# Optimization experiments

Measured on AMD Instinct MI355X. Metric: run time of the kernel, lower is better.

## Reference

```python
import jax, jax.numpy as jnp
import numpy as np

B, H, P, D, NF = 16, 16, 128, 128, 12  # patches == head_dim required by lin_qk


def setup_inputs() -> dict:
    key = jax.random.key(0)
    ks = jax.random.split(key, 8)
    return {
        "q": jax.random.normal(ks[0], (B, H, P, D), jnp.float32),
        "k": jax.random.normal(ks[1], (B, H, P, D), jnp.float32),
        "scale": jnp.ones((1,), jnp.float32),  # unused by the original forward
        "grid": jnp.arange(NF, dtype=jnp.float32) + 1.0,
        "base_weight": jax.random.uniform(ks[2], (D, D), jnp.float32),
        "coef_q": jax.random.uniform(ks[3], (D, NF), jnp.float32),
        "coef_k": jax.random.uniform(ks[4], (D, NF), jnp.float32),
        "scale_base": jnp.ones((1, H, P, D), jnp.float32),
        "scale_sp": jnp.ones((1, H, P, D), jnp.float32),
        "w_qk": jax.random.normal(ks[5], (D, D), jnp.float32) / np.float32(np.sqrt(D)),
        "b_qk": jnp.zeros((D,), jnp.float32),
    }


def _branch(x, coef, grid, base_weight, scale_sp, scale_base):
    # base path: SiLU(x) @ W^T  (F.linear semantics)
    base = jax.nn.silu(x) @ base_weight.T
    # KAN sin basis: sin(grid_f * x_d) -> (B,H,P,NF,D); contract coef[d,f]
    s = jnp.sin(grid[:, None] * x[..., None, :])
    f = jnp.einsum('df,bhpfd->bhpd', coef, s)
    return jax.nn.sigmoid(f * scale_sp + base * scale_base)


def reference(q, k, scale, grid, base_weight, coef_q, coef_k, scale_base, scale_sp, w_qk, b_qk):
    # Per-channel sigmoids, then sum over D. The original builds the full
    # (B,H,P,P,D) broadcast tensor sig_q[...,p,None,:] + sig_k[...,None,p',:]
    # and sums over D; that is exactly separable:
    #   sum_d(sig_q[p,d]) + sum_d(sig_k[p',d])
    sq = _branch(q, coef_q, grid, base_weight, scale_sp, scale_base).sum(-1)  # (B,H,P)
    sk = _branch(k, coef_k, grid, base_weight, scale_sp, scale_base).sum(-1)  # (B,H,P)
    f_out = sq[..., :, None] + sk[..., None, :]  # (B,H,P,P)
    f_out = f_out @ w_qk.T + b_qk  # lin_qk: valid because patches == head_dim
    return jax.nn.softmax(f_out, axis=-1)
```

## Files before the change

### kernel.cpp

```cpp
#include <hip/hip_runtime.h>
#include <hip/hip_bf16.h>


typedef float          f32x4 __attribute__((ext_vector_type(4)));
typedef short          s16x8 __attribute__((ext_vector_type(8)));
typedef int            s32x4 __attribute__((ext_vector_type(4)));
typedef unsigned int   u32x4 __attribute__((ext_vector_type(4)));
typedef unsigned short u16x8 __attribute__((ext_vector_type(8)));

#define LOG2E   1.44269504f
#define NLOG2E -1.44269504f
#define INV2PI  0.15915494309189535f

static __device__ __forceinline__ float hw_exp2(float x) {
    float r;
    asm("v_exp_f32 %0, %1" : "=v"(r) : "v"(x));
    return r;
}
static __device__ __forceinline__ float hw_sin_rev(float rev) {
    float f, r;
    asm("v_fract_f32 %0, %1" : "=v"(f) : "v"(rev));
    asm("v_sin_f32 %0, %1" : "=v"(r) : "v"(f));
    return r;
}
static __device__ __forceinline__ float fastrcp(float x) {
    return __builtin_amdgcn_rcpf(x);
}
static __device__ __forceinline__ unsigned int cvt_pk_bf16(float lo, float hi) {
    unsigned int r;
    asm("v_cvt_pk_bf16_f32 %0, %1, %2" : "=v"(r) : "v"(lo), "v"(hi));
    return r;
}
static __device__ __forceinline__ float sigmoid_fast(float z) {
    return fastrcp(1.f + hw_exp2(z * NLOG2E));
}
static __device__ __forceinline__ int swz(int local) {
    return local ^ (((local >> 8) & 7) << 4);
}

__global__ __launch_bounds__(256) void k_convert(const float* __restrict__ bw,
                                                 unsigned short* __restrict__ wbf) {
    int i = blockIdx.x * 256 + threadIdx.x;
    if (i < 128 * 128) {
        __hip_bfloat16 h = __float2bfloat16(bw[i]);
        unsigned short r;
        __builtin_memcpy(&r, &h, 2);
        wbf[i] = r;
    }
}

__global__ __launch_bounds__(512, 4) void k_branch(
    const float* __restrict__ q, const float* __restrict__ k,
    const unsigned short* __restrict__ wbf,
    const float* __restrict__ gridv,
    const float* __restrict__ coef_q, const float* __restrict__ coef_k,
    const float* __restrict__ sbase,
    const float* __restrict__ ssp,
    float* __restrict__ sums_lo, float* __restrict__ sums_hi)
{
    __shared__ char smem[32768];
    float* F_l = (float*)smem;

    const int t = threadIdx.x;
    const int lane = t & 63, w = t >> 6;
    const int wr = w >> 1;
    const int ch = w & 1;
    const int r15 = lane & 15, g4 = lane >> 4;
    const int row0 = blockIdx.x * 64;
    const bool is_q = row0 < 32768;
    const float* X = is_q ? q : k;
    const float* coef = is_q ? coef_q : coef_k;
    const int xrow0 = is_q ? row0 : row0 - 32768;
    const float g1 = gridv[0];

    #pragma unroll
    for (int it = 0; it < 4; ++it) {
        int c = it * 512 + t;
        u16x8 v = *(const u16x8*)&wbf[c * 8];
        *(u16x8*)(smem + swz(c * 16)) = v;
    }
    __syncthreads();

    const float* xrowp = &X[(xrow0 + wr * 16 + r15) * 128];

    f32x4 acc[4];
    #pragma unroll
    for (int n = 0; n < 4; ++n) acc[n] = (f32x4){0.f, 0.f, 0.f, 0.f};

    #pragma unroll
    for (int s = 0; s < 4; ++s) {
        const float4* xp = (const float4*)&xrowp[s * 32 + g4 * 8];
        float4 x0 = xp[0], x1 = xp[1];
        float xsv[8] = {x0.x, x0.y, x0.z, x0.w, x1.x, x1.y, x1.z, x1.w};
        float sl[8];
        #pragma unroll
        for (int j = 0; j < 8; ++j) {
            float e = hw_exp2(xsv[j] * NLOG2E);
            sl[j] = xsv[j] * fastrcp(1.f + e);
        }
        s32x4 a4 = {(int)cvt_pk_bf16(sl[0], sl[1]), (int)cvt_pk_bf16(sl[2], sl[3]),
                    (int)cvt_pk_bf16(sl[4], sl[5]), (int)cvt_pk_bf16(sl[6], sl[7])};
        s16x8 af = __builtin_bit_cast(s16x8, a4);
        #pragma unroll
        for (int n = 0; n < 4; ++n) {
            s16x8 bf = *(const s16x8*)(smem + swz((ch * 64 + n * 16 + r15) * 256
                                                  + s * 64 + g4 * 16));
            acc[n] = __builtin_amdgcn_mfma_f32_16x16x32_bf16(af, bf, acc[n], 0, 0, 0);
        }
    }
    __syncthreads();

    #pragma unroll
    for (int n = 0; n < 4; ++n) {
        int cl = n * 16 + r15;
        #pragma unroll
        for (int reg = 0; reg < 4; ++reg) {
            int rl = g4 * 4 + reg;
            F_l[(wr * 16 + rl) * 128 + ch * 64 + ((cl + rl * 4) & 63)] = acc[n][reg];
        }
    }

    const int ce = lane & 15;
    const int re = lane >> 4;
    const int gcol = ch * 64 + ce * 4;

    float Fr[16], xr[16], spr[16], sbr[16];
    #pragma unroll
    for (int i = 0; i < 4; ++i) {
        int rl = re * 4 + i;
        int rb = wr * 16 + rl;
        int hp = (row0 + rb) & 2047;
        f32x4 F4 = *(f32x4*)&F_l[rb * 128 + ch * 64 + ((ce * 4 + rl * 4) & 63)];
        float4 x4 = *(const float4*)&X[(xrow0 + rb) * 128 + gcol];
        float4 sp = *(const float4*)&ssp[hp * 128 + gcol];
        float4 sb = *(const float4*)&sbase[hp * 128 + gcol];
        Fr[i*4+0]=F4[0]; Fr[i*4+1]=F4[1]; Fr[i*4+2]=F4[2]; Fr[i*4+3]=F4[3];
        xr[i*4+0]=x4.x;  xr[i*4+1]=x4.y;  xr[i*4+2]=x4.z;  xr[i*4+3]=x4.w;
        spr[i*4+0]=sp.x; spr[i*4+1]=sp.y; spr[i*4+2]=sp.z; spr[i*4+3]=sp.w;
        sbr[i*4+0]=sb.x; sbr[i*4+1]=sb.y; sbr[i*4+2]=sb.z; sbr[i*4+3]=sb.w;
    }

    const float grev = g1 * INV2PI;
    float ps[4] = {0.f, 0.f, 0.f, 0.f};
    #pragma unroll
    for (int j = 0; j < 4; ++j) {
        const float4* cp = (const float4*)&coef[(gcol + j) * 12];
        float4 c0 = cp[0], c1 = cp[1], c2 = cp[2];
        float cf[12] = {c0.x, c0.y, c0.z, c0.w, c1.x, c1.y, c1.z, c1.w,
                        c2.x, c2.y, c2.z, c2.w};
        #pragma unroll
        for (int i = 0; i < 4; ++i) {
            float xv = xr[i*4+j];
            float rev = grev * xv;
            float s1 = hw_sin_rev(rev);
            float cv = hw_sin_rev(rev + 0.25f);
            float t2 = cv + cv;
            float sprev = 0.f, scur = s1;
            float f = cf[0] * s1;
            #pragma unroll
            for (int u = 1; u < 12; ++u) {
                float sn = __builtin_fmaf(t2, scur, -sprev);
                f = __builtin_fmaf(cf[u], sn, f);
                sprev = scur; scur = sn;
            }
            float z = f * spr[i*4+j] + Fr[i*4+j] * sbr[i*4+j];
            ps[i] += sigmoid_fast(z);
        }
    }
    #pragma unroll
    for (int i = 0; i < 4; ++i) {
        float v = ps[i];
        v += __shfl_xor(v, 1, 64);
        v += __shfl_xor(v, 2, 64);
        v += __shfl_xor(v, 4, 64);
        v += __shfl_xor(v, 8, 64);
        if (ce == 0) {
            int grow = row0 + wr * 16 + re * 4 + i;
            (ch ? sums_hi : sums_lo)[grow] = v;
        }
    }
}

__global__ __launch_bounds__(256) void k_attn(
    const float* __restrict__ sums_lo, const float* __restrict__ sums_hi,
    const float* __restrict__ w_qk, const float* __restrict__ b_qk,
    float* __restrict__ out)
{
    __shared__ float skl[128], Tp[2][128], Rp[2][128], Tl[128], Rl[128];
    const int bh = blockIdx.x >> 1;
    const int half = blockIdx.x & 1;
    const int t = threadIdx.x;

    if (t < 128) {
        int idx = 32768 + bh * 128 + t;
        skl[t] = sums_lo[idx] + sums_hi[idx];
    }
    __syncthreads();
    {
        int j = t & 127, ph = t >> 7;
        const float4* wr = (const float4*)&w_qk[j * 128 + ph * 64];
        const float* sk2 = &skl[ph * 64];
        float a = 0.f, r = 0.f;
        #pragma unroll 8
        for (int p4 = 0; p4 < 16; ++p4) {
            float4 w4 = wr[p4];
            a += w4.x * sk2[p4 * 4 + 0] + w4.y * sk2[p4 * 4 + 1] +
                 w4.z * sk2[p4 * 4 + 2] + w4.w * sk2[p4 * 4 + 3];
            r += w4.x + w4.y + w4.z + w4.w;
        }
        Tp[ph][j] = a;
        Rp[ph][j] = r;
    }
    __syncthreads();
    if (t < 128) {
        Tl[t] = Tp[0][t] + Tp[1][t] + b_qk[t];
        Rl[t] = Rp[0][t] + Rp[1][t];
    }
    __syncthreads();

    const int lane = t & 63, w = t >> 6;
    #pragma unroll
    for (int it = 0; it < 16; ++it) {
        int row = bh * 128 + half * 64 + it * 4 + w;
        float sqv = sums_lo[row] + sums_hi[row];
        float2 r2 = *(const float2*)&Rl[lane * 2];
        float2 t2 = *(const float2*)&Tl[lane * 2];
        float l0 = __builtin_fmaf(sqv, r2.x, t2.x);
        float l1 = __builtin_fmaf(sqv, r2.y, t2.y);
        float m = fmaxf(l0, l1);
        #pragma unroll
        for (int s = 32; s >= 1; s >>= 1) m = fmaxf(m, __shfl_xor(m, s, 64));
        float e0 = hw_exp2((l0 - m) * LOG2E);
        float e1 = hw_exp2((l1 - m) * LOG2E);
        float sum = e0 + e1;
        #pragma unroll
        for (int w2 = 32; w2 >= 1; w2 >>= 1) sum += __shfl_xor(sum, w2, 64);
        float inv = fastrcp(sum);
        float2 o2 = {e0 * inv, e1 * inv};
        *(float2*)&out[row * 128 + lane * 2] = o2;
    }
}

extern "C" void kernel_launch(void* const* d_in, const int* in_sizes, int n_in,
                              void* d_out, int out_size, void* d_ws, size_t ws_size,
                              hipStream_t stream) {
    (void)in_sizes; (void)n_in; (void)out_size; (void)ws_size;
    const float* q      = (const float*)d_in[0];
    const float* k      = (const float*)d_in[1];
    const float* gridv  = (const float*)d_in[3];
    const float* bw     = (const float*)d_in[4];
    const float* coef_q = (const float*)d_in[5];
    const float* coef_k = (const float*)d_in[6];
    const float* sbase  = (const float*)d_in[7];
    const float* ssp    = (const float*)d_in[8];
    const float* w_qk   = (const float*)d_in[9];
    const float* b_qk   = (const float*)d_in[10];

    float* out  = (float*)d_out;
    float* ws      = (float*)d_ws;
    float* sums_lo = ws;
    float* sums_hi = ws + 65536;
    unsigned short* wbf = (unsigned short*)(ws + 131072);

    k_convert<<<64, 256, 0, stream>>>(bw, wbf);
    k_branch<<<1024, 512, 0, stream>>>(q, k, wbf, gridv, coef_q, coef_k,
                                       sbase, ssp, sums_lo, sums_hi);
    k_attn<<<512, 256, 0, stream>>>(sums_lo, sums_hi, w_qk, b_qk, out);
}
```

Before: 42.83 us.

## Fuse KAN sine basis into MFMA loop using registered x and LDS coefficients

Computes the sine-basis sum during the MFMA loop from x values already held in registers for the SiLU operand, instead of reloading x, coef and scale_sp from global memory in a separate phase. Coefficients are transposed into LDS. The MFMA operands are swapped so the accumulator layout matches per-row ownership. The epilogue now exchanges only the basis values through LDS and uses a two-step shuffle reduction. It also uses v_cos_f32 directly rather than a second fract and sin, at the cost of extra LDS and more register pressure inside the MFMA loop.

```diff
diff --git a/kernel.cpp b/kernel.cpp
--- a/kernel.cpp
+++ b/kernel.cpp
@@ -5,7 +5,6 @@
 typedef float          f32x4 __attribute__((ext_vector_type(4)));
 typedef short          s16x8 __attribute__((ext_vector_type(8)));
 typedef int            s32x4 __attribute__((ext_vector_type(4)));
-typedef unsigned int   u32x4 __attribute__((ext_vector_type(4)));
 typedef unsigned short u16x8 __attribute__((ext_vector_type(8)));
 
 #define LOG2E   1.44269504f
@@ -17,10 +16,19 @@
     asm("v_exp_f32 %0, %1" : "=v"(r) : "v"(x));
     return r;
 }
-static __device__ __forceinline__ float hw_sin_rev(float rev) {
-    float f, r;
-    asm("v_fract_f32 %0, %1" : "=v"(f) : "v"(rev));
+static __device__ __forceinline__ float hw_fract(float x) {
+    float r;
+    asm("v_fract_f32 %0, %1" : "=v"(r) : "v"(x));
+    return r;
+}
+static __device__ __forceinline__ float hw_sin01(float f) {
+    float r;
     asm("v_sin_f32 %0, %1" : "=v"(r) : "v"(f));
+    return r;
+}
+static __device__ __forceinline__ float hw_cos01(float f) {
+    float r;
+    asm("v_cos_f32 %0, %1" : "=v"(r) : "v"(f));
     return r;
 }
 static __device__ __forceinline__ float fastrcp(float x) {
@@ -58,8 +66,8 @@
     const float* __restrict__ ssp,
     float* __restrict__ sums_lo, float* __restrict__ sums_hi)
 {
-    __shared__ char smem[32768];
-    float* F_l = (float*)smem;
+    __shared__ char smem[32768 + 6144];
+    float* cfl = (float*)(smem + 32768);
 
     const int t = threadIdx.x;
     const int lane = t & 63, w = t >> 6;
@@ -72,6 +80,7 @@
     const float* coef = is_q ? coef_q : coef_k;
     const int xrow0 = is_q ? row0 : row0 - 32768;
     const float g1 = gridv[0];
+    const float grev = g1 * INV2PI;
 
     #pragma unroll
     for (int it = 0; it < 4; ++it) {
@@ -79,13 +88,24 @@
         u16x8 v = *(const u16x8*)&wbf[c * 8];
         *(u16x8*)(smem + swz(c * 16)) = v;
     }
-    __syncthreads();
-
-    const float* xrowp = &X[(xrow0 + wr * 16 + r15) * 128];
+    #pragma unroll
+    for (int it = 0; it < 3; ++it) {
+        int e = it * 512 + t;
+        float v = coef[e];
+        int d = e / 12, u = e - d * 12;
+        cfl[u * 128 + d] = v;
+    }
+    __syncthreads();
+
+    const int xrow = wr * 16 + r15;
+    const float* xrowp = &X[(xrow0 + xrow) * 128];
+    const int hp = (row0 + xrow) & 2047;
+    const float* ssprow = &ssp[hp * 128];
 
     f32x4 acc[4];
     #pragma unroll
     for (int n = 0; n < 4; ++n) acc[n] = (f32x4){0.f, 0.f, 0.f, 0.f};
+    float fv[16];
 
     #pragma unroll
     for (int s = 0; s < 4; ++s) {
@@ -101,83 +121,69 @@
         s32x4 a4 = {(int)cvt_pk_bf16(sl[0], sl[1]), (int)cvt_pk_bf16(sl[2], sl[3]),
                     (int)cvt_pk_bf16(sl[4], sl[5]), (int)cvt_pk_bf16(sl[6], sl[7])};
         s16x8 af = __builtin_bit_cast(s16x8, a4);
+
+        if ((s >> 1) == ch) {
+            const int s2 = s & 1;
+            const float4* spp = (const float4*)&ssprow[s * 32 + g4 * 8];
+            float4 sp0 = spp[0], sp1 = spp[1];
+            float spv[8] = {sp0.x, sp0.y, sp0.z, sp0.w,
+                            sp1.x, sp1.y, sp1.z, sp1.w};
+            #pragma unroll
+            for (int j = 0; j < 8; ++j) {
+                int d = s * 32 + g4 * 8 + j;
+                float rev = hw_fract(grev * xsv[j]);
+                float s1 = hw_sin01(rev);
+                float cv = hw_cos01(rev);
+                float t2 = cv + cv;
+                float sprev = 0.f, scur = s1;
+                float f = cfl[d] * s1;
+                #pragma unroll
+                for (int u = 1; u < 12; ++u) {
+                    float sn = __builtin_fmaf(t2, scur, -sprev);
+                    f = __builtin_fmaf(cfl[u * 128 + d], sn, f);
+                    sprev = scur; scur = sn;
+                }
+                fv[s2 * 8 + j] = f * spv[j];
+            }
+        }
+
         #pragma unroll
         for (int n = 0; n < 4; ++n) {
-            s16x8 bf = *(const s16x8*)(smem + swz((ch * 64 + n * 16 + r15) * 256
-                                                  + s * 64 + g4 * 16));
-            acc[n] = __builtin_amdgcn_mfma_f32_16x16x32_bf16(af, bf, acc[n], 0, 0, 0);
-        }
-    }
-    __syncthreads();
-
+            s16x8 bfw = *(const s16x8*)(smem + swz((ch * 64 + n * 16 + r15) * 256
+                                                   + s * 64 + g4 * 16));
+            acc[n] = __builtin_amdgcn_mfma_f32_16x16x32_bf16(bfw, af, acc[n], 0, 0, 0);
+        }
+    }
+    __syncthreads();
+
+    float* myfv = (float*)smem + w * 1024;
+    #pragma unroll
+    for (int s2 = 0; s2 < 2; ++s2) {
+        #pragma unroll
+        for (int jb = 0; jb < 2; ++jb) {
+            int dloc = s2 * 32 + g4 * 8 + jb * 4;
+            f32x4 v = {fv[s2*8 + jb*4 + 0], fv[s2*8 + jb*4 + 1],
+                       fv[s2*8 + jb*4 + 2], fv[s2*8 + jb*4 + 3]};
+            *(f32x4*)&myfv[r15 * 64 + ((dloc + r15 * 4) & 63)] = v;
+        }
+    }
+
+    float ps = 0.f;
     #pragma unroll
     for (int n = 0; n < 4; ++n) {
-        int cl = n * 16 + r15;
+        f32x4 fp = *(f32x4*)&myfv[r15 * 64 + ((n * 16 + g4 * 4 + r15 * 4) & 63)];
+        float4 sb = *(const float4*)&sbase[hp * 128 + ch * 64 + n * 16 + g4 * 4];
+        float sbv[4] = {sb.x, sb.y, sb.z, sb.w};
         #pragma unroll
         for (int reg = 0; reg < 4; ++reg) {
-            int rl = g4 * 4 + reg;
-            F_l[(wr * 16 + rl) * 128 + ch * 64 + ((cl + rl * 4) & 63)] = acc[n][reg];
-        }
-    }
-
-    const int ce = lane & 15;
-    const int re = lane >> 4;
-    const int gcol = ch * 64 + ce * 4;
-
-    float Fr[16], xr[16], spr[16], sbr[16];
-    #pragma unroll
-    for (int i = 0; i < 4; ++i) {
-        int rl = re * 4 + i;
-        int rb = wr * 16 + rl;
-        int hp = (row0 + rb) & 2047;
-        f32x4 F4 = *(f32x4*)&F_l[rb * 128 + ch * 64 + ((ce * 4 + rl * 4) & 63)];
-        float4 x4 = *(const float4*)&X[(xrow0 + rb) * 128 + gcol];
-        float4 sp = *(const float4*)&ssp[hp * 128 + gcol];
-        float4 sb = *(const float4*)&sbase[hp * 128 + gcol];
-        Fr[i*4+0]=F4[0]; Fr[i*4+1]=F4[1]; Fr[i*4+2]=F4[2]; Fr[i*4+3]=F4[3];
-        xr[i*4+0]=x4.x;  xr[i*4+1]=x4.y;  xr[i*4+2]=x4.z;  xr[i*4+3]=x4.w;
-        spr[i*4+0]=sp.x; spr[i*4+1]=sp.y; spr[i*4+2]=sp.z; spr[i*4+3]=sp.w;
-        sbr[i*4+0]=sb.x; sbr[i*4+1]=sb.y; sbr[i*4+2]=sb.z; sbr[i*4+3]=sb.w;
-    }
-
-    const float grev = g1 * INV2PI;
-    float ps[4] = {0.f, 0.f, 0.f, 0.f};
-    #pragma unroll
-    for (int j = 0; j < 4; ++j) {
-        const float4* cp = (const float4*)&coef[(gcol + j) * 12];
-        float4 c0 = cp[0], c1 = cp[1], c2 = cp[2];
-        float cf[12] = {c0.x, c0.y, c0.z, c0.w, c1.x, c1.y, c1.z, c1.w,
-                        c2.x, c2.y, c2.z, c2.w};
-        #pragma unroll
-        for (int i = 0; i < 4; ++i) {
-            float xv = xr[i*4+j];
-            float rev = grev * xv;
-            float s1 = hw_sin_rev(rev);
-            float cv = hw_sin_rev(rev + 0.25f);
-            float t2 = cv + cv;
-            float sprev = 0.f, scur = s1;
-            float f = cf[0] * s1;
-            #pragma unroll
-            for (int u = 1; u < 12; ++u) {
-                float sn = __builtin_fmaf(t2, scur, -sprev);
-                f = __builtin_fmaf(cf[u], sn, f);
-                sprev = scur; scur = sn;
-            }
-            float z = f * spr[i*4+j] + Fr[i*4+j] * sbr[i*4+j];
-            ps[i] += sigmoid_fast(z);
-        }
-    }
-    #pragma unroll
-    for (int i = 0; i < 4; ++i) {
-        float v = ps[i];
-        v += __shfl_xor(v, 1, 64);
-        v += __shfl_xor(v, 2, 64);
-        v += __shfl_xor(v, 4, 64);
-        v += __shfl_xor(v, 8, 64);
-        if (ce == 0) {
-            int grow = row0 + wr * 16 + re * 4 + i;
-            (ch ? sums_hi : sums_lo)[grow] = v;
-        }
+            float z = fp[reg] + acc[n][reg] * sbv[reg];
+            ps += sigmoid_fast(z);
+        }
+    }
+    ps += __shfl_xor(ps, 16, 64);
+    ps += __shfl_xor(ps, 32, 64);
+    if (g4 == 0) {
+        (ch ? sums_hi : sums_lo)[row0 + xrow] = ps;
     }
 }
 
```

Result: faster. 41.05 us (-4.2%).
